# Kernel tuning notes

Measured on AMD Instinct MI355X. Metric: run time of the kernel, lower is better.

The kernel has to match this reference:

```python
import jax, jax.numpy as jnp
import numpy as np

EMBED_DIM = 512
N_HEADS = 8
HEAD_DIM = EMBED_DIM // N_HEADS
B, S = 4, 2048

def gelu(x):
    # torch F.gelu default = exact erf gelu
    return jax.nn.gelu(x, approximate=False)

def setup_inputs() -> dict:
    key = jax.random.key(0)
    ks = jax.random.split(key, 9)
    sc = 1.0 / np.sqrt(EMBED_DIM)
    inp = {
        'x':   jax.random.normal(ks[0], (B, S, EMBED_DIM), dtype=jnp.float32),
        'Wq':  jax.random.uniform(ks[1], (EMBED_DIM, EMBED_DIM), jnp.float32, -sc, sc),
        'bq':  jax.random.uniform(ks[2], (EMBED_DIM,), jnp.float32, -sc, sc),
        'Wk':  jax.random.uniform(ks[3], (EMBED_DIM, EMBED_DIM), jnp.float32, -sc, sc),
        'bk':  jax.random.uniform(ks[4], (EMBED_DIM,), jnp.float32, -sc, sc),
        'Wv':  jax.random.uniform(ks[5], (EMBED_DIM, EMBED_DIM), jnp.float32, -sc, sc),
        'bv':  jax.random.uniform(ks[6], (EMBED_DIM,), jnp.float32, -sc, sc),
        'Wo':  jax.random.uniform(ks[7], (EMBED_DIM, EMBED_DIM), jnp.float32, -sc, sc),
        'bo':  jax.random.uniform(ks[8], (EMBED_DIM,), jnp.float32, -sc, sc),
    }
    return inp

def reference(x, Wq, bq, Wk, bk, Wv, bv, Wo, bo):
    Bsz, Ssz, _ = x.shape
    def proj(W, b):
        # [B,S,E] -> [B,H,S,D], GELU applied before head split (same math either way)
        h = gelu(jnp.einsum('bse,ef->bsf', x, W.T) + b)
        return h.reshape(Bsz, Ssz, N_HEADS, HEAD_DIM).transpose(0, 2, 1, 3)
    q = proj(Wq, bq)
    k = proj(Wk, bk)
    v = proj(Wv, bv)
    attn = jnp.einsum('bhid,bhjd->bhij', q, k) / np.sqrt(HEAD_DIM).astype(np.float32)
    attn = jax.nn.softmax(attn, axis=-1)
    o = jnp.einsum('bhij,bhjd->bhid', attn, v)
    o = o.transpose(0, 2, 1, 3).reshape(Bsz, Ssz, EMBED_DIM)
    return gelu(jnp.einsum('bse,ef->bsf', o, Wo.T) + bo)
```

## Files before the change

### kernel.cpp

```cpp
#include <hip/hip_runtime.h>
#include <hip/hip_bf16.h>

typedef __bf16 bf16_t;
typedef __bf16 bf16x4 __attribute__((ext_vector_type(4)));
typedef __bf16 bf16x8 __attribute__((ext_vector_type(8)));
typedef float  f32x4  __attribute__((ext_vector_type(4)));
typedef float  f32x8  __attribute__((ext_vector_type(8)));

#define EMBED 512
#define NH    8
#define HD    64
#define SEQ   2048
#define MTOT  8192
#define SCQ   0.18033688011112042f

__device__ __forceinline__ float gelu_f(float x) {
    return 0.5f * x * (1.0f + erff(x * 0.7071067811865475f));
}

__device__ __forceinline__ f32x4 mfma16(bf16x8 a, bf16x8 b, f32x4 c) {
    return __builtin_amdgcn_mfma_f32_16x16x32_bf16(a, b, c, 0, 0, 0);
}

__global__ __launch_bounds__(256)
void convert_kernel(const float* __restrict__ x,  const float* __restrict__ Wq,
                    const float* __restrict__ Wk, const float* __restrict__ Wv,
                    bf16_t* __restrict__ xb, bf16_t* __restrict__ wb)
{
    const int y = blockIdx.y;
    const float* src; bf16_t* dst;
    if (y < 16)      { src = x + (size_t)y * 262144; dst = xb + (size_t)y * 262144; }
    else if (y == 16){ src = Wq; dst = wb; }
    else if (y == 17){ src = Wk; dst = wb + 262144; }
    else             { src = Wv; dst = wb + 524288; }
    const int base = (blockIdx.x * 256 + threadIdx.x) * 16;
    const f32x8 a = *(const f32x8*)(src + base);
    const f32x8 b = *(const f32x8*)(src + base + 8);
    *(bf16x8*)(dst + base)     = __builtin_convertvector(a, bf16x8);
    *(bf16x8*)(dst + base + 8) = __builtin_convertvector(b, bf16x8);
}

template<int MODE, int NTILE>
__global__ __launch_bounds__(256, 3)
void gemm_gelu_kernel(const bf16_t* __restrict__ Xb,
                      const bf16_t* __restrict__ Wb,
                      const float*  __restrict__ Wf,
                      const float*  __restrict__ Bq, const float* __restrict__ Bk,
                      const float*  __restrict__ Bv,
                      bf16_t* __restrict__ O0, bf16_t* __restrict__ O1,
                      bf16_t* __restrict__ O2, float* __restrict__ Of)
{
    constexpr int NTN = NTILE / 32;
    __shared__ __align__(16) bf16_t As[128 * 72];
    __shared__ __align__(16) bf16_t Bs[NTILE * 72];
    const int tid  = threadIdx.x;
    const int lane = tid & 63, w = tid >> 6, quad = lane >> 4, l15 = lane & 15;
    const int m0 = blockIdx.x * 128;
    int mat, n0;
    if (MODE == 0) { mat = blockIdx.y >> 2; n0 = (blockIdx.y & 3) * NTILE; }
    else           { mat = 0;               n0 = blockIdx.y * NTILE; }
    const bf16_t* W  = (MODE == 0) ? (Wb + (size_t)mat * 262144) : nullptr;
    const float*  Bi = (MODE == 1) ? Bq : (mat == 0 ? Bq : (mat == 1 ? Bk : Bv));

    const int wr = (w >> 1) * 64;
    const int wc = (w & 1) * (NTILE / 2);

    const int srow = tid >> 3, scol = (tid & 7) * 8;

    f32x4 acc[4][NTN];
#pragma unroll
    for (int a = 0; a < 4; ++a)
#pragma unroll
        for (int b = 0; b < NTN; ++b) acc[a][b] = f32x4{0.f, 0.f, 0.f, 0.f};

    bf16x8 xp[4];
    bf16x8 wpb[NTN];
    f32x8  wpf[NTN];

#pragma unroll
    for (int it = 0; it < 4; ++it)
        xp[it] = *(const bf16x8*)(Xb + (size_t)(m0 + it * 32 + srow) * EMBED + scol);
#pragma unroll
    for (int it = 0; it < NTN; ++it) {
        const int r = it * 32 + srow;
        if (MODE == 0) wpb[it] = *(const bf16x8*)(W + (size_t)(n0 + r) * EMBED + scol);
        else           wpf[it] = *(const f32x8*)(Wf + (size_t)(n0 + r) * EMBED + scol);
    }

#pragma unroll 1
    for (int kt = 0; kt < 8; ++kt) {
        __syncthreads();
#pragma unroll
        for (int it = 0; it < 4; ++it)
            *(bf16x8*)(As + (it * 32 + srow) * 72 + scol) = xp[it];
#pragma unroll
        for (int it = 0; it < NTN; ++it) {
            const int r = it * 32 + srow;
            if (MODE == 0) *(bf16x8*)(Bs + r * 72 + scol) = wpb[it];
            else *(bf16x8*)(Bs + r * 72 + scol) = __builtin_convertvector(wpf[it], bf16x8);
        }
        if (kt < 7) {
            const int k1 = (kt + 1) * 64;
#pragma unroll
            for (int it = 0; it < 4; ++it)
                xp[it] = *(const bf16x8*)(Xb + (size_t)(m0 + it * 32 + srow) * EMBED + k1 + scol);
#pragma unroll
            for (int it = 0; it < NTN; ++it) {
                const int r = it * 32 + srow;
                if (MODE == 0) wpb[it] = *(const bf16x8*)(W + (size_t)(n0 + r) * EMBED + k1 + scol);
                else           wpf[it] = *(const f32x8*)(Wf + (size_t)(n0 + r) * EMBED + k1 + scol);
            }
        }
        __syncthreads();
#pragma unroll
        for (int ks = 0; ks < 2; ++ks) {
            const int ko = (ks * 4 + quad) * 8;
            bf16x8 av[4], bv[NTN];
#pragma unroll
            for (int mt = 0; mt < 4; ++mt)
                av[mt] = *(const bf16x8*)(As + (wr + mt * 16 + l15) * 72 + ko);
#pragma unroll
            for (int nt = 0; nt < NTN; ++nt)
                bv[nt] = *(const bf16x8*)(Bs + (wc + nt * 16 + l15) * 72 + ko);
#pragma unroll
            for (int mt = 0; mt < 4; ++mt)
#pragma unroll
                for (int nt = 0; nt < NTN; ++nt)
                    acc[mt][nt] = mfma16(av[mt], bv[nt], acc[mt][nt]);
        }
    }

    float biasv[NTN];
#pragma unroll
    for (int nt = 0; nt < NTN; ++nt)
        biasv[nt] = Bi[n0 + wc + nt * 16 + l15];
#pragma unroll
    for (int mt = 0; mt < 4; ++mt) {
        const int mb = m0 + wr + mt * 16 + quad * 4;
        const int bb = mb >> 11, s0 = mb & (SEQ - 1);
#pragma unroll
        for (int nt = 0; nt < NTN; ++nt) {
            const int fc = n0 + wc + nt * 16 + l15;
            const int h = fc >> 6, d = fc & 63;
            float vv[4];
#pragma unroll
            for (int i = 0; i < 4; ++i) vv[i] = gelu_f(acc[mt][nt][i] + biasv[nt]);
            if (MODE == 1) {
#pragma unroll
                for (int i = 0; i < 4; ++i) Of[(size_t)(mb + i) * EMBED + fc] = vv[i];
            } else if (mat == 0) {
#pragma unroll
                for (int i = 0; i < 4; ++i)
                    O0[(((size_t)(bb * NH + h)) * SEQ + s0 + i) * HD + d] = (bf16_t)(vv[i] * SCQ);
            } else if (mat == 1) {
#pragma unroll
                for (int i = 0; i < 4; ++i)
                    O1[(((size_t)(bb * NH + h)) * SEQ + s0 + i) * HD + d] = (bf16_t)vv[i];
            } else {
                bf16x4 pk;
#pragma unroll
                for (int i = 0; i < 4; ++i) pk[i] = (bf16_t)vv[i];
                *(bf16x4*)(O2 + ((size_t)(bb * NH + h) * HD + d) * SEQ + s0) = pk;
            }
        }
    }
}

__global__ __launch_bounds__(256, 4)
void flash_attn_kernel(const bf16_t* __restrict__ Q,
                       const bf16_t* __restrict__ K,
                       const bf16_t* __restrict__ Vt,
                       bf16_t* __restrict__ Og)
{
    __shared__ __align__(16) bf16_t Ks[2][64 * 64];
    __shared__ __align__(16) bf16_t Vs[2][64 * 64];
    __shared__ __align__(16) bf16_t Ps[4][16 * 64];

    const int tid  = threadIdx.x;
    const int lane = tid & 63, w = tid >> 6, quad = lane >> 4, l15 = lane & 15;
    const int bh = blockIdx.y;
    const int q0 = blockIdx.x * 64;
    const size_t baseQK = (size_t)bh * SEQ * HD;
    const size_t baseV  = (size_t)bh * HD * SEQ;
    const int wm = w * 16;
    const int cx = (l15 & 7) << 3;

    bf16x8 qf[2];
#pragma unroll
    for (int ks = 0; ks < 2; ++ks)
        qf[ks] = *(const bf16x8*)(Q + baseQK + (size_t)(q0 + wm + l15) * HD + ks * 32 + quad * 8);

    f32x4 lacc = f32x4{0.f, 0.f, 0.f, 0.f};
    f32x4 oacc[4];
#pragma unroll
    for (int nt = 0; nt < 4; ++nt) oacc[nt] = f32x4{0.f, 0.f, 0.f, 0.f};

    bf16_t* Pw = Ps[w];
    const int r0 = tid >> 3, c0 = (tid & 7) * 8;
    const int sA = (r0 << 6) + (c0 ^ ((r0 & 7) << 3));
    bf16x8 kr0, kr1, vr0, vr1;

    kr0 = *(const bf16x8*)(K + baseQK + (size_t)r0 * HD + c0);
    kr1 = *(const bf16x8*)(K + baseQK + (size_t)(r0 + 32) * HD + c0);
    vr0 = *(const bf16x8*)(Vt + baseV + (size_t)r0 * SEQ + c0);
    vr1 = *(const bf16x8*)(Vt + baseV + (size_t)(r0 + 32) * SEQ + c0);
    *(bf16x8*)(Ks[0] + sA)        = kr0;
    *(bf16x8*)(Ks[0] + sA + 2048) = kr1;
    *(bf16x8*)(Vs[0] + sA)        = vr0;
    *(bf16x8*)(Vs[0] + sA + 2048) = vr1;
    kr0 = *(const bf16x8*)(K + baseQK + (size_t)(64 + r0) * HD + c0);
    kr1 = *(const bf16x8*)(K + baseQK + (size_t)(64 + r0 + 32) * HD + c0);
    vr0 = *(const bf16x8*)(Vt + baseV + (size_t)r0 * SEQ + 64 + c0);
    vr1 = *(const bf16x8*)(Vt + baseV + (size_t)(r0 + 32) * SEQ + 64 + c0);

#pragma unroll 1
    for (int t = 0; t < 32; ++t) {
        __syncthreads();
        if (t + 1 < 32) {
            bf16_t* Kn = Ks[(t + 1) & 1];
            bf16_t* Vn = Vs[(t + 1) & 1];
            *(bf16x8*)(Kn + sA)        = kr0;
            *(bf16x8*)(Kn + sA + 2048) = kr1;
            *(bf16x8*)(Vn + sA)        = vr0;
            *(bf16x8*)(Vn + sA + 2048) = vr1;
        }
        if (t + 2 < 32) {
            const int kv = (t + 2) * 64;
            kr0 = *(const bf16x8*)(K + baseQK + (size_t)(kv + r0) * HD + c0);
            kr1 = *(const bf16x8*)(K + baseQK + (size_t)(kv + r0 + 32) * HD + c0);
            vr0 = *(const bf16x8*)(Vt + baseV + (size_t)r0 * SEQ + kv + c0);
            vr1 = *(const bf16x8*)(Vt + baseV + (size_t)(r0 + 32) * SEQ + kv + c0);
        }

        const bf16_t* Kb = Ks[t & 1];
        const bf16_t* Vb = Vs[t & 1];

        f32x4 sf[4];
#pragma unroll
        for (int jt = 0; jt < 4; ++jt) sf[jt] = f32x4{0.f, 0.f, 0.f, 0.f};
        __builtin_amdgcn_s_setprio(1);
#pragma unroll
        for (int ks = 0; ks < 2; ++ks) {
            const int ko = (ks * 32 + quad * 8) ^ cx;
#pragma unroll
            for (int jt = 0; jt < 4; ++jt) {
                const bf16x8 a = *(const bf16x8*)(Kb + ((jt * 16 + l15) << 6) + ko);
                sf[jt] = mfma16(a, qf[ks], sf[jt]);
            }
        }
        __builtin_amdgcn_s_setprio(0);

#pragma unroll
        for (int jt = 0; jt < 4; ++jt) {
#pragma unroll
            for (int i = 0; i < 4; ++i) sf[jt][i] = exp2f(sf[jt][i] - 8.f);
            lacc += sf[jt];
            const bf16x4 pk = __builtin_convertvector(sf[jt], bf16x4);
            *(bf16x4*)(Pw + (l15 << 6) + ((jt * 16 + quad * 4) ^ cx)) = pk;
        }

        __builtin_amdgcn_s_setprio(1);
#pragma unroll
        for (int c = 0; c < 2; ++c) {
            const int ko = (c * 32 + quad * 8) ^ cx;
            const bf16x8 a = *(const bf16x8*)(Pw + (l15 << 6) + ko);
#pragma unroll
            for (int nt = 0; nt < 4; ++nt) {
                const bf16x8 b = *(const bf16x8*)(Vb + ((nt * 16 + l15) << 6) + ko);
                oacc[nt] = mfma16(a, b, oacc[nt]);
            }
        }
        __builtin_amdgcn_s_setprio(0);
    }

    float rs = (lacc[0] + lacc[1]) + (lacc[2] + lacc[3]);
    rs += __shfl_xor(rs, 16);
    rs += __shfl_xor(rs, 32);
    const int bidx = bh >> 3, h = bh & 7;
    float lf[4];
#pragma unroll
    for (int i = 0; i < 4; ++i)
        lf[i] = __shfl(rs, (lane & 48) | (quad * 4 + i));
#pragma unroll
    for (int nt = 0; nt < 4; ++nt)
#pragma unroll
        for (int i = 0; i < 4; ++i) {
            const int s = q0 + wm + quad * 4 + i;
            const int d = nt * 16 + l15;
            Og[((size_t)(bidx * SEQ + s)) * EMBED + h * HD + d] =
                (bf16_t)(oacc[nt][i] / lf[i]);
        }
}

extern "C" void kernel_launch(void* const* d_in, const int* in_sizes, int n_in,
                              void* d_out, int out_size, void* d_ws, size_t ws_size,
                              hipStream_t stream)
{
    const float* x  = (const float*)d_in[0];
    const float* Wq = (const float*)d_in[1];
    const float* bq = (const float*)d_in[2];
    const float* Wk = (const float*)d_in[3];
    const float* bk = (const float*)d_in[4];
    const float* Wv = (const float*)d_in[5];
    const float* bv = (const float*)d_in[6];
    const float* Wo = (const float*)d_in[7];
    const float* bo = (const float*)d_in[8];
    float* out = (float*)d_out;

    const size_t NE = (size_t)MTOT * EMBED;
    bf16_t* xb  = (bf16_t*)d_out;
    bf16_t* Qw  = (bf16_t*)d_out + NE;
    bf16_t* Kw  = (bf16_t*)d_ws;
    bf16_t* Vtw = Kw + NE;
    bf16_t* Ow  = Vtw + NE;
    bf16_t* Wb  = Ow;

    convert_kernel<<<dim3(64, 19), 256, 0, stream>>>(x, Wq, Wk, Wv, xb, Wb);
    gemm_gelu_kernel<0, 128><<<dim3(64, 12), 256, 0, stream>>>(
        xb, Wb, nullptr, bq, bk, bv, Qw, Kw, Vtw, nullptr);
    flash_attn_kernel<<<dim3(32, 32), 256, 0, stream>>>(Qw, Kw, Vtw, Ow);
    gemm_gelu_kernel<1, 64><<<dim3(64, 8), 256, 0, stream>>>(
        Ow, nullptr, Wo, bo, nullptr, nullptr, nullptr, nullptr, nullptr, out);
}
```

Baseline: 186.2 us.

## Process two 16-row query tiles per wave in flash attention to reuse K/V fragments

Each wave now handles 32 query rows instead of 16, so the block covers 128 queries and the grid halves. Every K and V fragment read from shared memory feeds two MFMAs, which halves LDS reads and global K/V traffic per query. The cost is more registers, so launch bounds drop to 2 blocks per CU, and the grid shrinks to 512 blocks, which may leave parts of the 256-CU device underused.

```diff
diff --git a/kernel.cpp b/kernel.cpp
--- a/kernel.cpp
+++ b/kernel.cpp
@@ -166,7 +166,7 @@
     }
 }
 
-__global__ __launch_bounds__(256, 4)
+__global__ __launch_bounds__(256, 2)
 void flash_attn_kernel(const bf16_t* __restrict__ Q,
                        const bf16_t* __restrict__ K,
                        const bf16_t* __restrict__ Vt,
@@ -174,28 +174,35 @@
 {
     __shared__ __align__(16) bf16_t Ks[2][64 * 64];
     __shared__ __align__(16) bf16_t Vs[2][64 * 64];
-    __shared__ __align__(16) bf16_t Ps[4][16 * 64];
+    __shared__ __align__(16) bf16_t Ps[4][2][16 * 64];
 
     const int tid  = threadIdx.x;
     const int lane = tid & 63, w = tid >> 6, quad = lane >> 4, l15 = lane & 15;
     const int bh = blockIdx.y;
-    const int q0 = blockIdx.x * 64;
+    const int q0 = blockIdx.x * 128;
     const size_t baseQK = (size_t)bh * SEQ * HD;
     const size_t baseV  = (size_t)bh * HD * SEQ;
-    const int wm = w * 16;
+    const int wm = w * 32;
     const int cx = (l15 & 7) << 3;
 
-    bf16x8 qf[2];
-#pragma unroll
-    for (int ks = 0; ks < 2; ++ks)
-        qf[ks] = *(const bf16x8*)(Q + baseQK + (size_t)(q0 + wm + l15) * HD + ks * 32 + quad * 8);
-
-    f32x4 lacc = f32x4{0.f, 0.f, 0.f, 0.f};
-    f32x4 oacc[4];
-#pragma unroll
-    for (int nt = 0; nt < 4; ++nt) oacc[nt] = f32x4{0.f, 0.f, 0.f, 0.f};
-
-    bf16_t* Pw = Ps[w];
+    bf16x8 qf0[2], qf1[2];
+#pragma unroll
+    for (int ks = 0; ks < 2; ++ks) {
+        qf0[ks] = *(const bf16x8*)(Q + baseQK + (size_t)(q0 + wm + l15) * HD + ks * 32 + quad * 8);
+        qf1[ks] = *(const bf16x8*)(Q + baseQK + (size_t)(q0 + wm + 16 + l15) * HD + ks * 32 + quad * 8);
+    }
+
+    f32x4 lacc0 = f32x4{0.f, 0.f, 0.f, 0.f};
+    f32x4 lacc1 = f32x4{0.f, 0.f, 0.f, 0.f};
+    f32x4 oacc0[4], oacc1[4];
+#pragma unroll
+    for (int nt = 0; nt < 4; ++nt) {
+        oacc0[nt] = f32x4{0.f, 0.f, 0.f, 0.f};
+        oacc1[nt] = f32x4{0.f, 0.f, 0.f, 0.f};
+    }
+
+    bf16_t* Pw0 = Ps[w][0];
+    bf16_t* Pw1 = Ps[w][1];
     const int r0 = tid >> 3, c0 = (tid & 7) * 8;
     const int sA = (r0 << 6) + (c0 ^ ((r0 & 7) << 3));
     bf16x8 kr0, kr1, vr0, vr1;
@@ -235,9 +242,12 @@
         const bf16_t* Kb = Ks[t & 1];
         const bf16_t* Vb = Vs[t & 1];
 
-        f32x4 sf[4];
-#pragma unroll
-        for (int jt = 0; jt < 4; ++jt) sf[jt] = f32x4{0.f, 0.f, 0.f, 0.f};
+        f32x4 sf0[4], sf1[4];
+#pragma unroll
+        for (int jt = 0; jt < 4; ++jt) {
+            sf0[jt] = f32x4{0.f, 0.f, 0.f, 0.f};
+            sf1[jt] = f32x4{0.f, 0.f, 0.f, 0.f};
+        }
         __builtin_amdgcn_s_setprio(1);
 #pragma unroll
         for (int ks = 0; ks < 2; ++ks) {
@@ -245,7 +255,8 @@
 #pragma unroll
             for (int jt = 0; jt < 4; ++jt) {
                 const bf16x8 a = *(const bf16x8*)(Kb + ((jt * 16 + l15) << 6) + ko);
-                sf[jt] = mfma16(a, qf[ks], sf[jt]);
+                sf0[jt] = mfma16(a, qf0[ks], sf0[jt]);
+                sf1[jt] = mfma16(a, qf1[ks], sf1[jt]);
             }
         }
         __builtin_amdgcn_s_setprio(0);
@@ -253,43 +264,58 @@
 #pragma unroll
         for (int jt = 0; jt < 4; ++jt) {
 #pragma unroll
-            for (int i = 0; i < 4; ++i) sf[jt][i] = exp2f(sf[jt][i] - 8.f);
-            lacc += sf[jt];
-            const bf16x4 pk = __builtin_convertvector(sf[jt], bf16x4);
-            *(bf16x4*)(Pw + (l15 << 6) + ((jt * 16 + quad * 4) ^ cx)) = pk;
+            for (int i = 0; i < 4; ++i) sf0[jt][i] = exp2f(sf0[jt][i] - 8.f);
+            lacc0 += sf0[jt];
+            const bf16x4 pk = __builtin_convertvector(sf0[jt], bf16x4);
+            *(bf16x4*)(Pw0 + (l15 << 6) + ((jt * 16 + quad * 4) ^ cx)) = pk;
+        }
+#pragma unroll
+        for (int jt = 0; jt < 4; ++jt) {
+#pragma unroll
+            for (int i = 0; i < 4; ++i) sf1[jt][i] = exp2f(sf1[jt][i] - 8.f);
+            lacc1 += sf1[jt];
+            const bf16x4 pk = __builtin_convertvector(sf1[jt], bf16x4);
+            *(bf16x4*)(Pw1 + (l15 << 6) + ((jt * 16 + quad * 4) ^ cx)) = pk;
         }
 
         __builtin_amdgcn_s_setprio(1);
 #pragma unroll
         for (int c = 0; c < 2; ++c) {
             const int ko = (c * 32 + quad * 8) ^ cx;
-            const bf16x8 a = *(const bf16x8*)(Pw + (l15 << 6) + ko);
+            const bf16x8 pa0 = *(const bf16x8*)(Pw0 + (l15 << 6) + ko);
+            const bf16x8 pa1 = *(const bf16x8*)(Pw1 + (l15 << 6) + ko);
 #pragma unroll
             for (int nt = 0; nt < 4; ++nt) {
                 const bf16x8 b = *(const bf16x8*)(Vb + ((nt * 16 + l15) << 6) + ko);
-                oacc[nt] = mfma16(a, b, oacc[nt]);
+                oacc0[nt] = mfma16(pa0, b, oacc0[nt]);
+                oacc1[nt] = mfma16(pa1, b, oacc1[nt]);
             }
         }
         __builtin_amdgcn_s_setprio(0);
     }
 
-    float rs = (lacc[0] + lacc[1]) + (lacc[2] + lacc[3]);
-    rs += __shfl_xor(rs, 16);
-    rs += __shfl_xor(rs, 32);
     const int bidx = bh >> 3, h = bh & 7;
-    float lf[4];
-#pragma unroll
-    for (int i = 0; i < 4; ++i)
-        lf[i] = __shfl(rs, (lane & 48) | (quad * 4 + i));
-#pragma unroll
-    for (int nt = 0; nt < 4; ++nt)
-#pragma unroll
-        for (int i = 0; i < 4; ++i) {
-            const int s = q0 + wm + quad * 4 + i;
-            const int d = nt * 16 + l15;
-            Og[((size_t)(bidx * SEQ + s)) * EMBED + h * HD + d] =
-                (bf16_t)(oacc[nt][i] / lf[i]);
-        }
+#pragma unroll
+    for (int g = 0; g < 2; ++g) {
+        const f32x4 la = g ? lacc1 : lacc0;
+        const f32x4* oa = g ? oacc1 : oacc0;
+        float rs = (la[0] + la[1]) + (la[2] + la[3]);
+        rs += __shfl_xor(rs, 16);
+        rs += __shfl_xor(rs, 32);
+        float lf[4];
+#pragma unroll
+        for (int i = 0; i < 4; ++i)
+            lf[i] = __shfl(rs, (lane & 48) | (quad * 4 + i));
+#pragma unroll
+        for (int nt = 0; nt < 4; ++nt)
+#pragma unroll
+            for (int i = 0; i < 4; ++i) {
+                const int s = q0 + wm + g * 16 + quad * 4 + i;
+                const int d = nt * 16 + l15;
+                Og[((size_t)(bidx * SEQ + s)) * EMBED + h * HD + d] =
+                    (bf16_t)(oa[nt][i] / lf[i]);
+            }
+    }
 }
 
 extern "C" void kernel_launch(void* const* d_in, const int* in_sizes, int n_in,
@@ -318,7 +344,7 @@
     convert_kernel<<<dim3(64, 19), 256, 0, stream>>>(x, Wq, Wk, Wv, xb, Wb);
     gemm_gelu_kernel<0, 128><<<dim3(64, 12), 256, 0, stream>>>(
         xb, Wb, nullptr, bq, bk, bv, Qw, Kw, Vtw, nullptr);
-    flash_attn_kernel<<<dim3(32, 32), 256, 0, stream>>>(Qw, Kw, Vtw, Ow);
+    flash_attn_kernel<<<dim3(16, 32), 256, 0, stream>>>(Qw, Kw, Vtw, Ow);
     gemm_gelu_kernel<1, 64><<<dim3(64, 8), 256, 0, stream>>>(
         Ow, nullptr, Wo, bo, nullptr, nullptr, nullptr, nullptr, nullptr, out);
 }
```

Result: no change. 185.3 us (-0.5%).
